# Performance work log

Hardware: AMD Instinct MI355X
Metric: run time of the kernel (lower is better)

The kernel has to match this reference:

```python
import jax, jax.numpy as jnp
import numpy as np

BATCH, SEQ, EMBED = 8, 1024, 2048
HEADS, LATENT = 16, 512
HEAD_DIM = EMBED // HEADS            # 128
NOPE = HEAD_DIM // 4                 # 32 (qk_rope_dim=96 is even, no adjust)
ROPE_D = HEAD_DIM - NOPE             # 96
THETA = 10000.0


def _rope_tables(seq_len):
    # matches torch: freqs over arange(0, rope_dim, 2)/rope_dim
    freqs = 1.0 / THETA ** (jnp.arange(0, ROPE_D, 2, dtype=jnp.float32) / ROPE_D)
    emb = jnp.arange(seq_len, dtype=jnp.float32)[:, None] * freqs[None, :]  # [S, ROPE_D//2]
    return jnp.cos(emb), jnp.sin(emb)


def _apply_rope(x, cos, sin):
    # x: [B,H,S,D]; cos/sin: [S,D//2]. NOTE: original concatenates halves (non-interleaved output).
    xe, xo = x[..., ::2], x[..., 1::2]
    return jnp.concatenate([xe * cos - xo * sin, xo * cos + xe * sin], axis=-1)


def setup_inputs() -> dict:
    key = jax.random.key(0)
    ks = jax.random.split(key, 5)
    x = jax.random.normal(ks[0], (BATCH, SEQ, EMBED), jnp.float32)
    Wq = jax.random.normal(ks[1], (EMBED, EMBED), jnp.float32) * 0.02
    Wkv_down = jax.random.normal(ks[2], (EMBED, LATENT), jnp.float32) * 0.02
    Wk_up = jax.random.normal(ks[3], (LATENT, EMBED), jnp.float32) * 0.02
    Wv_up = jax.random.normal(ks[4], (LATENT, EMBED), jnp.float32) * 0.02
    return {"x": x, "Wq": Wq, "Wkv_down": Wkv_down, "Wk_up": Wk_up, "Wv_up": Wv_up}


def reference(x, Wq, Wkv_down, Wk_up, Wv_up):
    B, S, E = x.shape
    # projections (weights stored [in, out], equivalent to nn.Linear math)
    q = (x @ Wq).reshape(B, S, HEADS, HEAD_DIM).transpose(0, 2, 1, 3)   # [B,H,S,D]
    q_nope, q_rope = q[..., :NOPE], q[..., NOPE:]
    c_kv = x @ Wkv_down                                                  # [B,S,latent]
    k = (c_kv @ Wk_up).reshape(B, S, HEADS, HEAD_DIM).transpose(0, 2, 1, 3)
    v = (c_kv @ Wv_up).reshape(B, S, HEADS, HEAD_DIM).transpose(0, 2, 1, 3)
    k_nope, k_rope = k[..., :NOPE], k[..., NOPE:]

    cos, sin = _rope_tables(S)
    q_rope = _apply_rope(q_rope, cos, sin)
    k_rope = _apply_rope(k_rope, cos, sin)

    qf = jnp.concatenate([q_nope, q_rope], axis=-1)
    kf = jnp.concatenate([k_nope, k_rope], axis=-1)

    scale = jnp.float32(1.0 / np.sqrt(HEAD_DIM))
    scores = jnp.einsum('bhqd,bhkd->bhqk', qf, kf) * scale
    causal = jnp.triu(jnp.ones((S, S), dtype=bool), k=1)  # past_length=0
    scores = jnp.where(causal, -jnp.inf, scores)
    weights = jax.nn.softmax(scores, axis=-1)
    out = jnp.einsum('bhqk,bhkd->bhqd', weights, v)
    return out.transpose(0, 2, 1, 3).reshape(B, S, E)
```

## Files before the change

kernel.cpp:

```cpp
#include <hip/hip_runtime.h>
#include <stdint.h>

typedef unsigned short u16;
typedef __bf16 bf16x8 __attribute__((ext_vector_type(8)));
typedef float    f32x4 __attribute__((ext_vector_type(4)));
typedef unsigned short u16x8 __attribute__((ext_vector_type(8)));

#define BB 8
#define SS 1024
#define EE 2048
#define HH 16
#define DD 128

__device__ __forceinline__ u16 f2bf(float f){
  union { float f; unsigned u; } v; v.f = f;
  unsigned r = v.u + 0x7FFFu + ((v.u >> 16) & 1u);
  return (u16)(r >> 16);
}
__device__ __forceinline__ float bf2f(u16 h){
  union { unsigned u; float f; } v; v.u = ((unsigned)h) << 16;
  return v.f;
}
__device__ __forceinline__ bf16x8 ld8(const u16* p){
  return __builtin_bit_cast(bf16x8, *(const u16x8*)p);
}

typedef __attribute__((address_space(1))) const unsigned int gas_u32;
typedef __attribute__((address_space(3))) unsigned int las_u32;
__device__ __forceinline__ void g2l16(const u16* g, u16* l){
  __builtin_amdgcn_global_load_lds((gas_u32*)g, (las_u32*)l, 16, 0, 0);
}

__global__ __launch_bounds__(256) void cvt_f32_bf16(const float* __restrict__ in,
                                                    u16* __restrict__ out, int n){
  int i = (blockIdx.x*256 + threadIdx.x)*8;
  if (i >= n) return;
  float4 v0 = *(const float4*)(in + i);
  float4 v1 = *(const float4*)(in + i + 4);
  u16x8 o;
  o[0]=f2bf(v0.x); o[1]=f2bf(v0.y); o[2]=f2bf(v0.z); o[3]=f2bf(v0.w);
  o[4]=f2bf(v1.x); o[5]=f2bf(v1.y); o[6]=f2bf(v1.z); o[7]=f2bf(v1.w);
  *(u16x8*)(out + i) = o;
}

__global__ __launch_bounds__(256) void transposeW(const float* __restrict__ W,
                                                  u16* __restrict__ Wt, int K, int N){
  __shared__ float t[32][33];
  int c = threadIdx.x & 31, r = threadIdx.x >> 5;
  int bx = blockIdx.x, by = blockIdx.y;
  #pragma unroll
  for (int i = 0; i < 32; i += 8)
    t[r+i][c] = W[(size_t)(by*32 + r + i)*N + bx*32 + c];
  __syncthreads();
  #pragma unroll
  for (int i = 0; i < 32; i += 8)
    Wt[(size_t)(bx*32 + r + i)*K + by*32 + c] = f2bf(t[c][r+i]);
}

__global__ __launch_bounds__(256) void rope_tables(float* __restrict__ cosb,
                                                   float* __restrict__ sinb){
  int i = blockIdx.x*256 + threadIdx.x;
  if (i >= SS*48) return;
  int s = i / 48, j = i % 48;
  float freq = powf(10000.0f, -((float)(2*j)) / 96.0f);
  float e = (float)s * freq;
  cosb[i] = cosf(e);
  sinb[i] = sinf(e);
}

__global__ __launch_bounds__(256) void rope_apply(u16* __restrict__ buf,
                                                  const float* __restrict__ cosb,
                                                  const float* __restrict__ sinb){
  int t = blockIdx.x*256 + threadIdx.x;
  int row = t >> 4, h = t & 15, s = row & (SS-1);
  u16* p = buf + (size_t)row*EE + h*DD + 32;
  float e[48], o[48];
  #pragma unroll
  for (int c = 0; c < 12; c++){
    u16x8 v = *(const u16x8*)(p + c*8);
    #pragma unroll
    for (int j = 0; j < 4; j++){
      e[c*4 + j] = bf2f(v[2*j]);
      o[c*4 + j] = bf2f(v[2*j+1]);
    }
  }
  u16 ob[96];
  #pragma unroll
  for (int j = 0; j < 48; j++){
    float cs = cosb[s*48 + j], sn = sinb[s*48 + j];
    ob[j]      = f2bf(e[j]*cs - o[j]*sn);
    ob[48 + j] = f2bf(o[j]*cs + e[j]*sn);
  }
  #pragma unroll
  for (int c = 0; c < 12; c++)
    *(u16x8*)(p + c*8) = *(const u16x8*)(ob + c*8);
}

__global__ __launch_bounds__(256) void gemm_bt(const u16* __restrict__ A,
    const u16* __restrict__ Bt, u16* __restrict__ C, int M, int N, int K){
  __shared__ u16 Al[128*32];
  __shared__ u16 Bl[128*32];
  const int tid = threadIdx.x;
  const int lane = tid & 63, w = tid >> 6;
  const int wr = w >> 1, wc = w & 1;
  const int l15 = lane & 15, l4 = lane >> 4;
  const int bm = blockIdx.y*128, bn = blockIdx.x*128;
  const int srow = tid >> 2;
  const int skc  = (tid & 3) * 8;
  const u16* ga = A  + (size_t)(bm + srow)*K + skc;
  const u16* gb = Bt + (size_t)(bn + srow)*K + skc;
  u16* la = Al + w*512;
  u16* lb = Bl + w*512;
  f32x4 acc[4][4] = {};
  for (int k0 = 0; k0 < K; k0 += 32){
    __syncthreads();
    g2l16(ga + k0,          la);
    g2l16(ga + 64*K + k0,   la + 2048);
    g2l16(gb + k0,          lb);
    g2l16(gb + 64*K + k0,   lb + 2048);
    __syncthreads();
    bf16x8 af[4], bfr[4];
    #pragma unroll
    for (int m = 0; m < 4; m++) af[m]  = ld8(Al + (wr*64 + m*16 + l15)*32 + l4*8);
    #pragma unroll
    for (int n = 0; n < 4; n++) bfr[n] = ld8(Bl + (wc*64 + n*16 + l15)*32 + l4*8);
    #pragma unroll
    for (int m = 0; m < 4; m++)
      #pragma unroll
      for (int n = 0; n < 4; n++)
        acc[m][n] = __builtin_amdgcn_mfma_f32_16x16x32_bf16(af[m], bfr[n], acc[m][n], 0, 0, 0);
  }
  #pragma unroll
  for (int m = 0; m < 4; m++)
    #pragma unroll
    for (int n = 0; n < 4; n++)
      #pragma unroll
      for (int r = 0; r < 4; r++){
        int row = bm + wr*64 + m*16 + l4*4 + r;
        int col = bn + wc*64 + n*16 + l15;
        C[(size_t)row*N + col] = f2bf(acc[m][n][r]);
      }
}

#define BARRIER() asm volatile("s_barrier" ::: "memory")
#define VMCNT4()  asm volatile("s_waitcnt vmcnt(4)" ::: "memory")

#define AFR(buf, mf, ks) ld8(&AL[buf][wr][((mf)*16 + l15)*64 + ((((ks)*4 + l4) ^ r7) << 3)])
#define BFR(buf, nf, ks) ld8(&BL[buf][wc>>1][(((wc&1)*64 + (nf)*16 + l15))*64 + ((((ks)*4 + l4) ^ r7) << 3)])

#define STAGE_A(buf, h, kt) stage2(aRow, (h), (kt), K, &AL[buf][h][0], wj0)
#define STAGE_B(buf, h, kt) stage2(bRow, (h), (kt), K, &BL[buf][h][0], wj0)

__device__ __forceinline__ void stage2(const u16* rowbase, int h, int kt, int K,
                                       u16* lds, int wj0){
  const u16* g = rowbase + (size_t)h*128*K + kt*64;
  g2l16(g,               lds + wj0*512);
  g2l16(g + (size_t)8*K, lds + wj0*512 + 512);
}

#define PHASE(buf, q, LOADB, STAGE, VM) do{                                        \
  bf16x8 a00 = AFR(buf, 2*(q)  , 0);                                              \
  bf16x8 a01 = AFR(buf, 2*(q)  , 1);                                              \
  bf16x8 a10 = AFR(buf, 2*(q)+1, 0);                                              \
  bf16x8 a11 = AFR(buf, 2*(q)+1, 1);                                              \
  if (LOADB){                                                                      \
    _Pragma("unroll")                                                              \
    for (int nf = 0; nf < 4; nf++){ bq[nf][0]=BFR(buf,nf,0); bq[nf][1]=BFR(buf,nf,1); } \
  }                                                                                \
  STAGE;                                                                           \
  if (VM) VMCNT4();                                                                \
  BARRIER();                                                                       \
  __builtin_amdgcn_s_setprio(1);                                                   \
  _Pragma("unroll")                                                                \
  for (int nf = 0; nf < 4; nf++){                                                  \
    acc[2*(q)][nf]   = __builtin_amdgcn_mfma_f32_16x16x32_bf16(a00, bq[nf][0], acc[2*(q)][nf],0,0,0);   \
    acc[2*(q)+1][nf] = __builtin_amdgcn_mfma_f32_16x16x32_bf16(a10, bq[nf][0], acc[2*(q)+1][nf],0,0,0); \
  }                                                                                \
  _Pragma("unroll")                                                                \
  for (int nf = 0; nf < 4; nf++){                                                  \
    acc[2*(q)][nf]   = __builtin_amdgcn_mfma_f32_16x16x32_bf16(a01, bq[nf][1], acc[2*(q)][nf],0,0,0);   \
    acc[2*(q)+1][nf] = __builtin_amdgcn_mfma_f32_16x16x32_bf16(a11, bq[nf][1], acc[2*(q)+1][nf],0,0,0); \
  }                                                                                \
  __builtin_amdgcn_s_setprio(0);                                                   \
  BARRIER();                                                                       \
  __builtin_amdgcn_sched_barrier(0);                                               \
}while(0)

__global__ __launch_bounds__(512, 2) void gemm8(const u16* __restrict__ A,
    const u16* __restrict__ Bt, u16* __restrict__ C0, u16* __restrict__ C1,
    int K, int Nout, int nsplit){
  __shared__ u16 AL[2][2][128*64];
  __shared__ u16 BL[2][2][128*64];
  const int tid = threadIdx.x, lane = tid & 63, w = tid >> 6;
  const int wr = w >> 2, wc = w & 3;
  const int l15 = lane & 15, l4 = lane >> 4;
  const int r7 = l15 & 7;
  const int bm = blockIdx.y*256, bn = blockIdx.x*256;
  const int wj0 = w*2;
  const int cswz = (lane & 7) ^ (lane >> 3);
  const u16* aRow = A  + (size_t)(bm + wj0*8 + (lane>>3))*K + cswz*8;
  const u16* bRow = Bt + (size_t)(bn + wj0*8 + (lane>>3))*K + cswz*8;

  const int nkt = K >> 6;
  const int niter = nkt >> 1;

  STAGE_A(0, 0, 0); STAGE_A(0, 1, 0);
  STAGE_B(0, 0, 0); STAGE_B(0, 1, 0);
  STAGE_B(1, 0, 1); STAGE_B(1, 1, 1);
  VMCNT4();
  BARRIER();

  f32x4 acc[8][4] = {};
  bf16x8 bq[4][2];

  for (int it = 0; it < niter; ++it){
    const int kto = 2*it + 1;
    int kt2 = 2*it + 2; if (kt2 >= nkt) kt2 -= nkt;
    int kt3 = 2*it + 3; if (kt3 >= nkt) kt3 -= nkt;
    PHASE(0, 0, 1, STAGE_A(1, 0, kto), 0);
    PHASE(0, 1, 0, STAGE_A(1, 1, kto), 0);
    PHASE(0, 2, 0, STAGE_B(0, 0, kt2), 0);
    PHASE(0, 3, 0, STAGE_B(0, 1, kt2), 1);
    PHASE(1, 0, 1, STAGE_A(0, 0, kt2), 0);
    PHASE(1, 1, 0, STAGE_A(0, 1, kt2), 0);
    PHASE(1, 2, 0, STAGE_B(1, 0, kt3), 0);
    PHASE(1, 3, 0, STAGE_B(1, 1, kt3), 1);
  }
  asm volatile("s_waitcnt vmcnt(0)" ::: "memory");

  u16* Cd = (bn < nsplit) ? C0 : C1;
  const int bcol = (bn < nsplit) ? bn : bn - nsplit;
  #pragma unroll
  for (int mf = 0; mf < 8; mf++)
    #pragma unroll
    for (int nf = 0; nf < 4; nf++)
      #pragma unroll
      for (int r = 0; r < 4; r++){
        int row = bm + wr*128 + mf*16 + l4*4 + r;
        int col = bcol + wc*64 + nf*16 + l15;
        Cd[(size_t)row*Nout + col] = f2bf(acc[mf][nf][r]);
      }
}

#define KLD 136

__global__ __launch_bounds__(512) void attn(const u16* __restrict__ qp,
                                            const u16* __restrict__ kp,
                                            const u16* __restrict__ vp,
                                            float* __restrict__ out){
  __shared__ u16 Kl[64*KLD];
  __shared__ u16 Vt[128*64];
  __shared__ u16 Pl[8][16*72];
  const int tid = threadIdx.x, lane = tid & 63, w = tid >> 6;
  const int l15 = lane & 15, l4 = lane >> 4;
  const int qt = 7 - blockIdx.y;
  const int bh = blockIdx.x;
  const int b = bh >> 4, h = bh & 15;
  const int qbase = qt*128;
  const int qmin = qbase + w*16;
  const int srow = tid >> 3, sseg = tid & 7, d0 = sseg*16;
  const float c = 0.12751920700948998f;

  const size_t rowq = (size_t)(b*SS + qmin + l15)*EE + h*DD;
  bf16x8 qf[4];
  #pragma unroll
  for (int kk = 0; kk < 4; kk++) qf[kk] = ld8(qp + rowq + kk*32 + l4*8);

  f32x4 ao[8] = {};
  float mi[4], li[4];
  #pragma unroll
  for (int r = 0; r < 4; r++){ mi[r] = -3e38f; li[r] = 0.0f; }

  const int ntiles = 2*qt + 2;
  const int cb = ((srow >> 3) ^ ((sseg*2) & 7)) & 7;
  u16x8 kr0, kr1, vr0, vr1;
  {
    const u16* kg = kp + (size_t)(b*SS + srow)*EE + h*DD + d0;
    const u16* vg = vp + (size_t)(b*SS + srow)*EE + h*DD + d0;
    kr0 = *(const u16x8*)kg;     kr1 = *(const u16x8*)(kg + 8);
    vr0 = *(const u16x8*)vg;     vr1 = *(const u16x8*)(vg + 8);
  }

  for (int t = 0; t < ntiles; t++){
    const int kv0 = t*64;
    __syncthreads();
    *(u16x8*)(Kl + srow*KLD + d0)     = kr0;
    *(u16x8*)(Kl + srow*KLD + d0 + 8) = kr1;
    {
      u16* vbase = Vt + (size_t)d0*64 + (srow & 7);
      #pragma unroll
      for (int j = 0; j < 16; j++){
        int chunk = (cb ^ (j & 7) ^ (j >> 3)) & 7;
        u16 val = (j < 8) ? vr0[j] : vr1[j - 8];
        vbase[j*64 + chunk*8] = val;
      }
    }
    __syncthreads();
    if (t + 1 < ntiles){
      const u16* kg = kp + (size_t)(b*SS + kv0 + 64 + srow)*EE + h*DD + d0;
      const u16* vg = vp + (size_t)(b*SS + kv0 + 64 + srow)*EE + h*DD + d0;
      kr0 = *(const u16x8*)kg;   kr1 = *(const u16x8*)(kg + 8);
      vr0 = *(const u16x8*)vg;   vr1 = *(const u16x8*)(vg + 8);
    }
    if (kv0 <= qmin + 15){
      float sv[4][4];
      #pragma unroll
      for (int nt = 0; nt < 4; nt++){
        f32x4 sacc = {};
        #pragma unroll
        for (int kk = 0; kk < 4; kk++){
          bf16x8 kf = ld8(Kl + (nt*16 + l15)*KLD + kk*32 + l4*8);
          sacc = __builtin_amdgcn_mfma_f32_16x16x32_bf16(qf[kk], kf, sacc, 0, 0, 0);
        }
        #pragma unroll
        for (int r = 0; r < 4; r++) sv[nt][r] = sacc[r];
      }
      if (kv0 + 63 > qmin){
        #pragma unroll
        for (int nt = 0; nt < 4; nt++)
          #pragma unroll
          for (int r = 0; r < 4; r++){
            int qg = qmin + l4*4 + r;
            int kg_ = kv0 + nt*16 + l15;
            if (kg_ > qg) sv[nt][r] = -3e38f;
          }
      }
      float pout[4][4];
      #pragma unroll
      for (int r = 0; r < 4; r++){
        float mx = fmaxf(fmaxf(sv[0][r], sv[1][r]), fmaxf(sv[2][r], sv[3][r]));
        #pragma unroll
        for (int off = 1; off < 16; off <<= 1) mx = fmaxf(mx, __shfl_xor(mx, off));
        float mnew = fmaxf(mi[r], mx);
        float mnc = mnew * c;
        float alpha = __builtin_amdgcn_exp2f(__builtin_fmaf(mi[r], c, -mnc));
        float rs = 0.0f;
        #pragma unroll
        for (int nt = 0; nt < 4; nt++){
          float pv = __builtin_amdgcn_exp2f(__builtin_fmaf(sv[nt][r], c, -mnc));
          pout[nt][r] = pv; rs += pv;
        }
        #pragma unroll
        for (int off = 1; off < 16; off <<= 1) rs += __shfl_xor(rs, off);
        li[r] = li[r]*alpha + rs;
        mi[r] = mnew;
        #pragma unroll
        for (int n8 = 0; n8 < 8; n8++) ao[n8][r] *= alpha;
      }
      #pragma unroll
      for (int nt = 0; nt < 4; nt++)
        #pragma unroll
        for (int r = 0; r < 4; r++)
          Pl[w][(l4*4 + r)*72 + nt*16 + l15] = f2bf(pout[nt][r]);
      #pragma unroll
      for (int kk = 0; kk < 2; kk++){
        bf16x8 pa = ld8(&Pl[w][l15*72 + kk*32 + l4*8]);
        #pragma unroll
        for (int n8 = 0; n8 < 8; n8++){
          int d = n8*16 + l15;
          int kvc = kk*4 + l4;
          int chunk = (kvc ^ (d & 7) ^ ((d >> 3) & 7)) & 7;
          bf16x8 vf = ld8(Vt + d*64 + chunk*8);
          ao[n8] = __builtin_amdgcn_mfma_f32_16x16x32_bf16(pa, vf, ao[n8], 0, 0, 0);
        }
      }
    }
  }

  #pragma unroll
  for (int r = 0; r < 4; r++){
    float inv = 1.0f / li[r];
    size_t orow = (size_t)(b*SS + qmin + l4*4 + r)*EE + h*DD;
    #pragma unroll
    for (int n8 = 0; n8 < 8; n8++)
      out[orow + n8*16 + l15] = ao[n8][r]*inv;
  }
}

extern "C" void kernel_launch(void* const* d_in, const int* in_sizes, int n_in,
                              void* d_out, int out_size, void* d_ws, size_t ws_size,
                              hipStream_t stream){
  const float* x    = (const float*)d_in[0];
  const float* Wq   = (const float*)d_in[1];
  const float* Wkvd = (const float*)d_in[2];
  const float* Wku  = (const float*)d_in[3];
  const float* Wvu  = (const float*)d_in[4];
  float* out = (float*)d_out;
  char* ws = (char*)d_ws;

  u16*   xb    = (u16*)  (ws);
  u16*   WqT   = (u16*)  (ws +  33554432);
  u16*   WkvdT = (u16*)  (ws +  41943040);
  u16*   WkuT  = (u16*)  (ws +  44040192);
  u16*   WvuT  = (u16*)  (ws +  46137344);
  float* cosb  = (float*)(ws +  48234496);
  float* sinb  = (float*)(ws +  48431104);
  u16*   qp    = (u16*)  (ws +  48627712);
  u16*   ckv   = (u16*)  (ws +  82182144);
  u16*   kp    = (u16*)  (ws +  90570752);
  u16*   vp    = (u16*)  (ws + 124125184);

  cvt_f32_bf16<<<(BB*SS*EE)/(256*8), 256, 0, stream>>>(x, xb, BB*SS*EE);
  transposeW<<<dim3(EE/32,  EE/32), 256, 0, stream>>>(Wq,   WqT,   EE,  EE);
  transposeW<<<dim3(512/32, EE/32), 256, 0, stream>>>(Wkvd, WkvdT, EE,  512);
  transposeW<<<dim3(EE/32, 512/32), 256, 0, stream>>>(Wku,  WkuT,  512, EE);
  transposeW<<<dim3(EE/32, 512/32), 256, 0, stream>>>(Wvu,  WvuT,  512, EE);
  rope_tables<<<(SS*48 + 255)/256, 256, 0, stream>>>(cosb, sinb);

  gemm8<<<dim3(EE/256, (BB*SS)/256), 512, 0, stream>>>(xb, WqT, qp, qp, EE, EE, EE);
  gemm_bt<<<dim3(512/128, (BB*SS)/128), 256, 0, stream>>>(xb, WkvdT, ckv, BB*SS, 512, EE);
  gemm8<<<dim3(4096/256, (BB*SS)/256), 512, 0, stream>>>(ckv, WkuT, kp, vp, 512, EE, EE);

  rope_apply<<<(BB*SS*HH)/256, 256, 0, stream>>>(qp, cosb, sinb);
  rope_apply<<<(BB*SS*HH)/256, 256, 0, stream>>>(kp, cosb, sinb);

  attn<<<dim3(BB*HH, SS/128), 512, 0, stream>>>(qp, kp, vp, out);
}
```

Before: 334.9 us.

## Store V transposed from GEMM epilogue and stream K/V via async LDS loads

The K/V up-projection GEMM now writes V directly in a per-head transposed [B,H,D,S] layout. The attention kernel can then load V tiles with direct global-to-LDS copies instead of scattering transposed elements through registers. K tiles are double-buffered in LDS and prefetched asynchronously with XOR-swizzled addressing, with waitcnt and barriers placed so loads overlap compute. The cost is an uncoalesced-ish 4-element strided store in the GEMM epilogue and extra barriers per tile.

```diff
diff --git a/kernel.cpp b/kernel.cpp
--- a/kernel.cpp
+++ b/kernel.cpp
@@ -5,6 +5,7 @@
 typedef __bf16 bf16x8 __attribute__((ext_vector_type(8)));
 typedef float    f32x4 __attribute__((ext_vector_type(4)));
 typedef unsigned short u16x8 __attribute__((ext_vector_type(8)));
+typedef unsigned short u16x4 __attribute__((ext_vector_type(4)));
 
 #define BB 8
 #define SS 1024
@@ -30,6 +31,9 @@
 __device__ __forceinline__ void g2l16(const u16* g, u16* l){
   __builtin_amdgcn_global_load_lds((gas_u32*)g, (las_u32*)l, 16, 0, 0);
 }
+
+#define BARRIER() asm volatile("s_barrier" ::: "memory")
+#define VMC(n)    asm volatile("s_waitcnt vmcnt(" #n ")" ::: "memory")
 
 __global__ __launch_bounds__(256) void cvt_f32_bf16(const float* __restrict__ in,
                                                     u16* __restrict__ out, int n){
@@ -142,9 +146,6 @@
       }
 }
 
-#define BARRIER() asm volatile("s_barrier" ::: "memory")
-#define VMCNT4()  asm volatile("s_waitcnt vmcnt(4)" ::: "memory")
-
 #define AFR(buf, mf, ks) ld8(&AL[buf][wr][((mf)*16 + l15)*64 + ((((ks)*4 + l4) ^ r7) << 3)])
 #define BFR(buf, nf, ks) ld8(&BL[buf][wc>>1][(((wc&1)*64 + (nf)*16 + l15))*64 + ((((ks)*4 + l4) ^ r7) << 3)])
 
@@ -168,7 +169,7 @@
     for (int nf = 0; nf < 4; nf++){ bq[nf][0]=BFR(buf,nf,0); bq[nf][1]=BFR(buf,nf,1); } \
   }                                                                                \
   STAGE;                                                                           \
-  if (VM) VMCNT4();                                                                \
+  if (VM) VMC(4);                                                                  \
   BARRIER();                                                                       \
   __builtin_amdgcn_s_setprio(1);                                                   \
   _Pragma("unroll")                                                                \
@@ -188,7 +189,7 @@
 
 __global__ __launch_bounds__(512, 2) void gemm8(const u16* __restrict__ A,
     const u16* __restrict__ Bt, u16* __restrict__ C0, u16* __restrict__ C1,
-    int K, int Nout, int nsplit){
+    int K, int Nout, int nsplit, int vt){
   __shared__ u16 AL[2][2][128*64];
   __shared__ u16 BL[2][2][128*64];
   const int tid = threadIdx.x, lane = tid & 63, w = tid >> 6;
@@ -207,7 +208,7 @@
   STAGE_A(0, 0, 0); STAGE_A(0, 1, 0);
   STAGE_B(0, 0, 0); STAGE_B(0, 1, 0);
   STAGE_B(1, 0, 1); STAGE_B(1, 1, 1);
-  VMCNT4();
+  VMC(4);
   BARRIER();
 
   f32x4 acc[8][4] = {};
@@ -228,28 +229,44 @@
   }
   asm volatile("s_waitcnt vmcnt(0)" ::: "memory");
 
-  u16* Cd = (bn < nsplit) ? C0 : C1;
-  const int bcol = (bn < nsplit) ? bn : bn - nsplit;
-  #pragma unroll
-  for (int mf = 0; mf < 8; mf++)
-    #pragma unroll
-    for (int nf = 0; nf < 4; nf++)
-      #pragma unroll
-      for (int r = 0; r < 4; r++){
-        int row = bm + wr*128 + mf*16 + l4*4 + r;
-        int col = bcol + wc*64 + nf*16 + l15;
-        Cd[(size_t)row*Nout + col] = f2bf(acc[mf][nf][r]);
-      }
-}
-
-#define KLD 136
+  if (vt && bn >= nsplit){
+    const int bcol = bn - nsplit;
+    #pragma unroll
+    for (int mf = 0; mf < 8; mf++)
+      #pragma unroll
+      for (int nf = 0; nf < 4; nf++){
+        int row0 = bm + wr*128 + mf*16 + l4*4;
+        int col  = bcol + wc*64 + nf*16 + l15;
+        int bh = (row0 >> 10)*16 + (col >> 7);
+        int d  = col & 127;
+        int s  = row0 & 1023;
+        u16x4 pk;
+        #pragma unroll
+        for (int r = 0; r < 4; r++) pk[r] = f2bf(acc[mf][nf][r]);
+        *(u16x4*)(C1 + (((size_t)(bh*128 + d)) << 10) + s) = pk;
+      }
+  } else {
+    u16* Cd = (bn < nsplit) ? C0 : C1;
+    const int bcol = (bn < nsplit) ? bn : bn - nsplit;
+    #pragma unroll
+    for (int mf = 0; mf < 8; mf++)
+      #pragma unroll
+      for (int nf = 0; nf < 4; nf++)
+        #pragma unroll
+        for (int r = 0; r < 4; r++){
+          int row = bm + wr*128 + mf*16 + l4*4 + r;
+          int col = bcol + wc*64 + nf*16 + l15;
+          Cd[(size_t)row*Nout + col] = f2bf(acc[mf][nf][r]);
+        }
+  }
+}
 
 __global__ __launch_bounds__(512) void attn(const u16* __restrict__ qp,
                                             const u16* __restrict__ kp,
-                                            const u16* __restrict__ vp,
+                                            const u16* __restrict__ vpT,
                                             float* __restrict__ out){
-  __shared__ u16 Kl[64*KLD];
-  __shared__ u16 Vt[128*64];
+  __shared__ u16 Kl[2][64*128];
+  __shared__ u16 Vl[128*64];
   __shared__ u16 Pl[8][16*72];
   const int tid = threadIdx.x, lane = tid & 63, w = tid >> 6;
   const int l15 = lane & 15, l4 = lane >> 4;
@@ -258,13 +275,15 @@
   const int b = bh >> 4, h = bh & 15;
   const int qbase = qt*128;
   const int qmin = qbase + w*16;
-  const int srow = tid >> 3, sseg = tid & 7, d0 = sseg*16;
   const float c = 0.12751920700948998f;
 
+  const int kR0 = w*8 + (l4 & 3) + ((lane>>4)==0 ? 0 : 0);
   const size_t rowq = (size_t)(b*SS + qmin + l15)*EE + h*DD;
   bf16x8 qf[4];
   #pragma unroll
   for (int kk = 0; kk < 4; kk++) qf[kk] = ld8(qp + rowq + kk*32 + l4*8);
+  #pragma unroll
+  for (int kk = 0; kk < 4; kk++) asm volatile("" : "+v"(qf[kk]));
 
   f32x4 ao[8] = {};
   float mi[4], li[4];
@@ -272,44 +291,50 @@
   for (int r = 0; r < 4; r++){ mi[r] = -3e38f; li[r] = 0.0f; }
 
   const int ntiles = 2*qt + 2;
-  const int cb = ((srow >> 3) ^ ((sseg*2) & 7)) & 7;
-  u16x8 kr0, kr1, vr0, vr1;
-  {
-    const u16* kg = kp + (size_t)(b*SS + srow)*EE + h*DD + d0;
-    const u16* vg = vp + (size_t)(b*SS + srow)*EE + h*DD + d0;
-    kr0 = *(const u16x8*)kg;     kr1 = *(const u16x8*)(kg + 8);
-    vr0 = *(const u16x8*)vg;     vr1 = *(const u16x8*)(vg + 8);
-  }
+
+  #pragma unroll
+  for (int q = 0; q < 2; q++){
+    int r = w*8 + q*4 + (lane>>4);
+    int p = lane & 15;
+    g2l16(kp + (size_t)(b*SS + r)*EE + h*DD + ((p ^ (r&7))<<3),
+          &Kl[0][0] + (w*128 + q*64)*8);
+  }
+  VMC(0);
 
   for (int t = 0; t < ntiles; t++){
     const int kv0 = t*64;
-    __syncthreads();
-    *(u16x8*)(Kl + srow*KLD + d0)     = kr0;
-    *(u16x8*)(Kl + srow*KLD + d0 + 8) = kr1;
-    {
-      u16* vbase = Vt + (size_t)d0*64 + (srow & 7);
-      #pragma unroll
-      for (int j = 0; j < 16; j++){
-        int chunk = (cb ^ (j & 7) ^ (j >> 3)) & 7;
-        u16 val = (j < 8) ? vr0[j] : vr1[j - 8];
-        vbase[j*64 + chunk*8] = val;
-      }
+    const int buf = t & 1;
+    #pragma unroll
+    for (int q = 0; q < 2; q++){
+      int d = w*16 + q*8 + (lane>>3);
+      int cc = lane & 7;
+      g2l16(vpT + (size_t)(bh*DD + d)*SS + kv0 + ((cc ^ (d&7))<<3),
+            &Vl[0] + (w*128 + q*64)*8);
     }
-    __syncthreads();
     if (t + 1 < ntiles){
-      const u16* kg = kp + (size_t)(b*SS + kv0 + 64 + srow)*EE + h*DD + d0;
-      const u16* vg = vp + (size_t)(b*SS + kv0 + 64 + srow)*EE + h*DD + d0;
-      kr0 = *(const u16x8*)kg;   kr1 = *(const u16x8*)(kg + 8);
-      vr0 = *(const u16x8*)vg;   vr1 = *(const u16x8*)(vg + 8);
+      #pragma unroll
+      for (int q = 0; q < 2; q++){
+        int r = w*8 + q*4 + (lane>>4);
+        int p = lane & 15;
+        g2l16(kp + (size_t)(b*SS + kv0 + 64 + r)*EE + h*DD + ((p ^ (r&7))<<3),
+              &Kl[buf^1][0] + (w*128 + q*64)*8);
+      }
+      VMC(4);
+    } else {
+      VMC(2);
     }
-    if (kv0 <= qmin + 15){
+    BARRIER();
+
+    const bool part = (kv0 <= qmin + 15);
+    float pout[4][4];
+    if (part){
       float sv[4][4];
       #pragma unroll
       for (int nt = 0; nt < 4; nt++){
         f32x4 sacc = {};
         #pragma unroll
         for (int kk = 0; kk < 4; kk++){
-          bf16x8 kf = ld8(Kl + (nt*16 + l15)*KLD + kk*32 + l4*8);
+          bf16x8 kf = ld8(&Kl[buf][0] + (nt*16 + l15)*128 + (((kk*4 + l4) ^ (l15&7))<<3));
           sacc = __builtin_amdgcn_mfma_f32_16x16x32_bf16(qf[kk], kf, sacc, 0, 0, 0);
         }
         #pragma unroll
@@ -325,7 +350,6 @@
             if (kg_ > qg) sv[nt][r] = -3e38f;
           }
       }
-      float pout[4][4];
       #pragma unroll
       for (int r = 0; r < 4; r++){
         float mx = fmaxf(fmaxf(sv[0][r], sv[1][r]), fmaxf(sv[2][r], sv[3][r]));
@@ -352,19 +376,21 @@
         #pragma unroll
         for (int r = 0; r < 4; r++)
           Pl[w][(l4*4 + r)*72 + nt*16 + l15] = f2bf(pout[nt][r]);
+    }
+    if (t + 1 < ntiles) VMC(2); else VMC(0);
+    BARRIER();
+    if (part){
       #pragma unroll
       for (int kk = 0; kk < 2; kk++){
         bf16x8 pa = ld8(&Pl[w][l15*72 + kk*32 + l4*8]);
         #pragma unroll
         for (int n8 = 0; n8 < 8; n8++){
-          int d = n8*16 + l15;
-          int kvc = kk*4 + l4;
-          int chunk = (kvc ^ (d & 7) ^ ((d >> 3) & 7)) & 7;
-          bf16x8 vf = ld8(Vt + d*64 + chunk*8);
+          bf16x8 vf = ld8(&Vl[0] + (n8*16 + l15)*64 + (((kk*4 + l4) ^ (l15&7))<<3));
           ao[n8] = __builtin_amdgcn_mfma_f32_16x16x32_bf16(pa, vf, ao[n8], 0, 0, 0);
         }
       }
     }
+    BARRIER();
   }
 
   #pragma unroll
@@ -398,7 +424,7 @@
   u16*   qp    = (u16*)  (ws +  48627712);
   u16*   ckv   = (u16*)  (ws +  82182144);
   u16*   kp    = (u16*)  (ws +  90570752);
-  u16*   vp    = (u16*)  (ws + 124125184);
+  u16*   vpT   = (u16*)  (ws + 124125184);
 
   cvt_f32_bf16<<<(BB*SS*EE)/(256*8), 256, 0, stream>>>(x, xb, BB*SS*EE);
   transposeW<<<dim3(EE/32,  EE/32), 256, 0, stream>>>(Wq,   WqT,   EE,  EE);
@@ -407,12 +433,12 @@
   transposeW<<<dim3(EE/32, 512/32), 256, 0, stream>>>(Wvu,  WvuT,  512, EE);
   rope_tables<<<(SS*48 + 255)/256, 256, 0, stream>>>(cosb, sinb);
 
-  gemm8<<<dim3(EE/256, (BB*SS)/256), 512, 0, stream>>>(xb, WqT, qp, qp, EE, EE, EE);
+  gemm8<<<dim3(EE/256, (BB*SS)/256), 512, 0, stream>>>(xb, WqT, qp, qp, EE, EE, EE, 0);
   gemm_bt<<<dim3(512/128, (BB*SS)/128), 256, 0, stream>>>(xb, WkvdT, ckv, BB*SS, 512, EE);
-  gemm8<<<dim3(4096/256, (BB*SS)/256), 512, 0, stream>>>(ckv, WkuT, kp, vp, 512, EE, EE);
+  gemm8<<<dim3(4096/256, (BB*SS)/256), 512, 0, stream>>>(ckv, WkuT, kp, vpT, 512, EE, EE, 1);
 
   rope_apply<<<(BB*SS*HH)/256, 256, 0, stream>>>(qp, cosb, sinb);
   rope_apply<<<(BB*SS*HH)/256, 256, 0, stream>>>(kp, cosb, sinb);
 
-  attn<<<dim3(BB*HH, SS/128), 512, 0, stream>>>(qp, kp, vp, out);
-}
+  attn<<<dim3(BB*HH, SS/128), 512, 0, stream>>>(qp, kp, vpT, out);
+}
```

After: 325.7 us. -2.7%, faster.
